# Kernel tuning notes

Hardware: AMD Instinct MI355X
Metric: run time of the kernel (lower is better)

## Reference

```python
import jax, jax.numpy as jnp
from jax import lax
import numpy as np

MARKER_NUM = 50000
E = 256          # embed_dim
D = 512          # d_model
K = 16           # sample_size / neighbor_num
B = 128
S = 128
BETA = 0.1
MAX_TIME = 1000.0


def setup_inputs() -> dict:
    key = jax.random.key(0)
    ks = jax.random.split(key, 12)
    def lin(k, fan_in, shape):
        return (jax.random.normal(k, shape, jnp.float32) / np.sqrt(fan_in)).astype(jnp.float32)
    return {
        "marker_data": jax.random.randint(ks[0], (B, S), 0, MARKER_NUM),
        "time_data": jax.random.uniform(ks[1], (B, S), jnp.float32),
        "mask_data": jnp.ones((B, S), jnp.float32),
        "embedding": jax.random.normal(ks[2], (MARKER_NUM, E), jnp.float32) * 0.05,
        "neighbor_list": jax.random.randint(ks[3], (MARKER_NUM, K), 0, MARKER_NUM),
        "neighbor_prob": jax.random.uniform(ks[4], (MARKER_NUM, K), jnp.float32),
        "W_te": lin(ks[5], 1, (1, E)), "b_te": jnp.zeros((E,), jnp.float32),
        "W_el": lin(ks[6], E, (E, D)), "b_el": jnp.zeros((D,), jnp.float32),
        "W_ih": lin(ks[7], D, (D, D)), "b_ih": jnp.zeros((D,), jnp.float32),
        "W_hh": lin(ks[8], D, (D, D)), "b_hh": jnp.zeros((D,), jnp.float32),
        "W_time": lin(ks[9], D, (D, 1)), "b_time": jnp.zeros((1,), jnp.float32),
        "W_mk": lin(ks[10], E + D, (E + D, 1)), "b_mk": jnp.zeros((1,), jnp.float32),
    }


def reference(marker_data, time_data, mask_data, embedding, neighbor_list, neighbor_prob,
              W_te, b_te, W_el, b_el, W_ih, b_ih, W_hh, b_hh, W_time, b_time, W_mk, b_mk):
    leaky = lambda x: jnp.where(x >= 0, x, 0.01 * x)  # LeakyReLU(0.01)
    Bn, Sn = marker_data.shape
    L = 1 + (Sn - 1) * (K - 1)  # final candidate_list / prob_list width
    R = 1 + (Sn - 1) * K        # final neighbor_prob_record width

    cand0 = jnp.zeros((Bn, L), jnp.int32).at[:, 0].set(marker_data[:, 0].astype(jnp.int32))
    prob0 = jnp.zeros((Bn, L), jnp.float32).at[:, 0].set(1.0)  # zero pad -> never sampled
    nrec0 = jnp.ones((Bn, R), jnp.float32)
    chosen0 = jnp.zeros((Bn, 1), jnp.int32)
    h0 = jnp.zeros((Bn, D), jnp.float32)
    carry0 = (h0, time_data[:, 0:1], marker_data[:, 0:1].astype(jnp.int32), cand0, prob0, nrec0, chosen0)
    keys = jax.random.split(jax.random.key(42), Sn - 1)

    def step(carry, xt):
        t, key = xt
        h, last_t, last_m, cand, prob, nrec, chosen = carry
        # embedding of (marker, time)
        time_emb = last_t @ W_te + b_te                       # (B,E)
        vec = embedding[last_m[:, 0]] + BETA * time_emb       # (B,E)
        x = leaky(vec @ W_el + b_el)                          # (B,D)
        # single-layer tanh RNN step (nn.RNN)
        h = jnp.tanh(x @ W_ih + b_ih + h @ W_hh + b_hh)
        new_t = last_t + jax.nn.softplus(h @ W_time + b_time)  # (B,1)
        new_mask = (new_t < MAX_TIME).astype(jnp.float32)
        # sampled neighbors of last marker
        neigh = neighbor_list[last_m[:, 0]].astype(jnp.int32)  # (B,K)
        p_neigh = neighbor_prob[last_m[:, 0]]                  # (B,K)
        nrec = lax.dynamic_update_slice(nrec, p_neigh, (0, 1 + t * K))
        inf = jnp.concatenate([embedding[neigh], jnp.broadcast_to(h[:, None, :], (Bn, K, D))], axis=-1)
        mprob = jax.nn.softmax((inf @ W_mk + b_mk)[..., 0], axis=1)  # (B,K)
        cand = lax.dynamic_update_slice(cand, neigh[:, 1:], (0, 1 + t * (K - 1)))
        chosen_p = jnp.take_along_axis(prob, chosen, 1)        # (B,1)
        attached = chosen_p * mprob                            # (B,K)
        prob = prob.at[jnp.arange(Bn), chosen[:, 0]].set(attached[:, 0])
        prob = lax.dynamic_update_slice(prob, attached[:, 1:], (0, 1 + t * (K - 1)))
        # torch.multinomial(prob_list, 1) == categorical over normalized probs
        logits = jnp.where(prob > 0, jnp.log(jnp.maximum(prob, 1e-38)), -1e30)
        new_chosen = jax.random.categorical(key, lax.stop_gradient(logits), axis=1)[:, None].astype(jnp.int32)
        new_m = jnp.take_along_axis(cand, new_chosen, 1)       # (B,1)
        sel_np = jnp.take_along_axis(nrec, new_chosen, 1)
        sel_sp = jnp.take_along_axis(prob, new_chosen, 1)
        new_carry = (h, new_t, new_m, cand, prob, nrec, new_chosen)
        return new_carry, (new_m[:, 0], new_t[:, 0], new_mask[:, 0], sel_np[:, 0], sel_sp[:, 0])

    _, (ms, ts, mk, nps, sps) = lax.scan(step, carry0, (jnp.arange(Sn - 1), keys))
    ones = jnp.ones((Bn, 1), jnp.float32)
    marker_res = jnp.concatenate([marker_data[:, 0:1].astype(jnp.int32), ms.T], axis=1)
    time_res = jnp.concatenate([time_data[:, 0:1], ts.T], axis=1)
    mask_res = jnp.concatenate([mask_data[:, 0:1], mk.T], axis=1)
    total_neighbor_prob = jnp.concatenate([ones, nps.T], axis=1)
    total_sample_prob = jnp.concatenate([ones, sps.T], axis=1)
    return (marker_res, time_res, mask_res, total_neighbor_prob, total_sample_prob)
```

## Files before the change

### kernel.cpp

```cpp
#include <hip/hip_runtime.h>
#include <stdint.h>
#include <stddef.h>

#define BB 128
#define SS 128
#define EE 256
#define DD 512
#define KK 16
#define LL 1906
#define RR 2033
#define NSTEP 127

static __device__ __forceinline__ uint32_t rotl32(uint32_t v, int r) {
  return (v << r) | (v >> (32 - r));
}

static __device__ __forceinline__ void tf2x32(uint32_t k0, uint32_t k1,
                                              uint32_t x0, uint32_t x1,
                                              uint32_t &o0, uint32_t &o1) {
  uint32_t ks2 = k0 ^ k1 ^ 0x1BD11BDAu;
  x0 += k0; x1 += k1;
#define TFR(r) { x0 += x1; x1 = rotl32(x1, (r)); x1 ^= x0; }
  TFR(13) TFR(15) TFR(26) TFR(6)
  x0 += k1;  x1 += ks2 + 1u;
  TFR(17) TFR(29) TFR(16) TFR(24)
  x0 += ks2; x1 += k0 + 2u;
  TFR(13) TFR(15) TFR(26) TFR(6)
  x0 += k0;  x1 += k1 + 3u;
  TFR(17) TFR(29) TFR(16) TFR(24)
  x0 += k1;  x1 += ks2 + 4u;
  TFR(13) TFR(15) TFR(26) TFR(6)
  x0 += ks2; x1 += k0 + 5u;
#undef TFR
  o0 = x0; o1 = x1;
}

static __device__ __forceinline__ float jax_gumbel(uint32_t bits) {
  float f = __uint_as_float((bits >> 9) | 0x3F800000u) - 1.0f;
  float u = fmaxf(f, 1.17549435e-38f);
  return -logf(-logf(u));
}

__global__ __launch_bounds__(1024) void rnn_gen_kernel(
    const int*   __restrict__ marker_data,
    const float* __restrict__ time_data,
    const float* __restrict__ mask_data,
    const float* __restrict__ embedding,
    const int*   __restrict__ neighbor_list,
    const float* __restrict__ neighbor_prob,
    const float* __restrict__ W_te,
    const float* __restrict__ b_te,
    const float* __restrict__ W_el,
    const float* __restrict__ b_el,
    const float* __restrict__ W_ih,
    const float* __restrict__ b_ih,
    const float* __restrict__ W_hh,
    const float* __restrict__ b_hh,
    const float* __restrict__ W_time,
    const float* __restrict__ b_time,
    const float* __restrict__ W_mk,
    const float* __restrict__ b_mk,
    float* __restrict__ out)
{
  __shared__ float  s_prob[LL];
  __shared__ int    s_cand[LL];
  __shared__ float  s_nrec[RR];
  __shared__ float  s_x[DD];
  __shared__ float  s_h[DD];
  __shared__ float  s_vec[EE];
  __shared__ double s_pd[8][DD];
  __shared__ double s_edot[KK];
  __shared__ double s_rt[8];
  __shared__ double s_rm[8];
  __shared__ float  s_red_z[16];
  __shared__ int    s_red_i[16];
  __shared__ int    s_neigh[KK];
  __shared__ float  s_last_t;
  __shared__ int    s_last_m;
  __shared__ int    s_chosen;
  __shared__ float  s_newt;
  __shared__ uint32_t s_k0, s_k1;

  const int b   = blockIdx.x;
  const int tid = threadIdx.x;

  for (int i = tid; i < LL; i += 1024) { s_prob[i] = 0.0f; s_cand[i] = 0; }
  for (int i = tid; i < RR; i += 1024) s_nrec[i] = 1.0f;
  if (tid < DD) s_h[tid] = 0.0f;
  if (tid == 0) {
    int   m0 = marker_data[b * SS];
    float t0 = time_data[b * SS];
    s_cand[0] = m0; s_prob[0] = 1.0f;
    s_last_m = m0; s_last_t = t0; s_chosen = 0;
    out[0 * BB * SS + b * SS + 0] = (float)m0;
    out[1 * BB * SS + b * SS + 0] = t0;
    out[2 * BB * SS + b * SS + 0] = mask_data[b * SS];
    out[3 * BB * SS + b * SS + 0] = 1.0f;
    out[4 * BB * SS + b * SS + 0] = 1.0f;
  }
  __syncthreads();

  for (int t = 0; t < NSTEP; ++t) {
    const int   m  = s_last_m;
    const float lt = s_last_t;

    if (tid == 768) {
      uint32_t o0, o1;
      tf2x32(0u, 42u, 0u, (uint32_t)t, o0, o1);
      s_k0 = o0; s_k1 = o1;
    }
    if (tid < EE) {
      float te = __fadd_rn(__fmul_rn(lt, W_te[tid]), b_te[tid]);
      s_vec[tid] = __fadd_rn(embedding[(size_t)m * EE + tid], __fmul_rn(0.1f, te));
    }
    if (tid >= 256 && tid < 256 + KK) {
      int k = tid - 256;
      int nb = neighbor_list[(size_t)m * KK + k];
      s_neigh[k] = nb;
      s_nrec[1 + t * KK + k] = neighbor_prob[(size_t)m * KK + k];
      if (k >= 1) s_cand[1 + t * (KK - 1) + (k - 1)] = nb;
    }
    __syncthreads();

    float4 ev0 = make_float4(0.f,0.f,0.f,0.f), ev1 = ev0;
    if (tid >= 512) {
      int k = (tid - 512) >> 5, l32 = tid & 31;
      const float4* er = (const float4*)(embedding + (size_t)s_neigh[k] * EE);
      ev0 = er[2 * l32]; ev1 = er[2 * l32 + 1];
    }
    {
      const int jg = tid & 127;
      const int i0 = (tid >> 7) << 5;
      const float4* W4 = (const float4*)W_el + (size_t)i0 * 128 + jg;
      double d0 = 0.0, d1 = 0.0, d2 = 0.0, d3 = 0.0;
#pragma unroll 4
      for (int i = 0; i < 32; i += 4) {
        float4 a4 = *(const float4*)&s_vec[i0 + i];
        float4 w0 = W4[0], w1 = W4[128], w2 = W4[256], w3 = W4[384];
        W4 += 512;
        d0 = fma((double)a4.x, (double)w0.x, d0); d1 = fma((double)a4.x, (double)w0.y, d1);
        d2 = fma((double)a4.x, (double)w0.z, d2); d3 = fma((double)a4.x, (double)w0.w, d3);
        d0 = fma((double)a4.y, (double)w1.x, d0); d1 = fma((double)a4.y, (double)w1.y, d1);
        d2 = fma((double)a4.y, (double)w1.z, d2); d3 = fma((double)a4.y, (double)w1.w, d3);
        d0 = fma((double)a4.z, (double)w2.x, d0); d1 = fma((double)a4.z, (double)w2.y, d1);
        d2 = fma((double)a4.z, (double)w2.z, d2); d3 = fma((double)a4.z, (double)w2.w, d3);
        d0 = fma((double)a4.w, (double)w3.x, d0); d1 = fma((double)a4.w, (double)w3.y, d1);
        d2 = fma((double)a4.w, (double)w3.z, d2); d3 = fma((double)a4.w, (double)w3.w, d3);
      }
      double* pd = &s_pd[tid >> 7][4 * jg];
      pd[0] = d0; pd[1] = d1; pd[2] = d2; pd[3] = d3;
    }
    __syncthreads();

    if (tid < DD) {
      double d = ((s_pd[0][tid] + s_pd[1][tid]) + (s_pd[2][tid] + s_pd[3][tid]))
               + ((s_pd[4][tid] + s_pd[5][tid]) + (s_pd[6][tid] + s_pd[7][tid]));
      float z = __fadd_rn((float)d, b_el[tid]);
      s_x[tid] = (z >= 0.0f) ? z : __fmul_rn(0.01f, z);
    }
    __syncthreads();

    {
      const int tl = tid & 511;
      const int jg = tl & 127;
      const int i0 = (tl >> 7) << 7;
      const float*  av = (tid < 512) ? s_x : s_h;
      const float*  Wm = (tid < 512) ? W_ih : W_hh;
      const float4* W4 = (const float4*)Wm + (size_t)i0 * 128 + jg;
      double d0 = 0.0, d1 = 0.0, d2 = 0.0, d3 = 0.0;
#pragma unroll 4
      for (int i = 0; i < 128; i += 4) {
        float4 a4 = *(const float4*)&av[i0 + i];
        float4 w0 = W4[0], w1 = W4[128], w2 = W4[256], w3 = W4[384];
        W4 += 512;
        d0 = fma((double)a4.x, (double)w0.x, d0); d1 = fma((double)a4.x, (double)w0.y, d1);
        d2 = fma((double)a4.x, (double)w0.z, d2); d3 = fma((double)a4.x, (double)w0.w, d3);
        d0 = fma((double)a4.y, (double)w1.x, d0); d1 = fma((double)a4.y, (double)w1.y, d1);
        d2 = fma((double)a4.y, (double)w1.z, d2); d3 = fma((double)a4.y, (double)w1.w, d3);
        d0 = fma((double)a4.z, (double)w2.x, d0); d1 = fma((double)a4.z, (double)w2.y, d1);
        d2 = fma((double)a4.z, (double)w2.z, d2); d3 = fma((double)a4.z, (double)w2.w, d3);
        d0 = fma((double)a4.w, (double)w3.x, d0); d1 = fma((double)a4.w, (double)w3.y, d1);
        d2 = fma((double)a4.w, (double)w3.z, d2); d3 = fma((double)a4.w, (double)w3.w, d3);
      }
      double* pd = &s_pd[tid >> 7][4 * jg];
      pd[0] = d0; pd[1] = d1; pd[2] = d2; pd[3] = d3;
    }
    __syncthreads();

    if (tid < DD) {
      double ih = (s_pd[0][tid] + s_pd[1][tid]) + (s_pd[2][tid] + s_pd[3][tid]);
      double hh = (s_pd[4][tid] + s_pd[5][tid]) + (s_pd[6][tid] + s_pd[7][tid]);
      float p = __fadd_rn(__fadd_rn(__fadd_rn((float)ih, b_ih[tid]), (float)hh), b_hh[tid]);
      s_h[tid] = (float)tanh((double)p);
    }
    __syncthreads();

    if (tid < DD) {
      double hv = (double)s_h[tid];
      double pt = hv * (double)W_time[tid];
      double pm = hv * (double)W_mk[EE + tid];
      for (int off = 32; off > 0; off >>= 1) {
        pt += __shfl_down(pt, off);
        pm += __shfl_down(pm, off);
      }
      if ((tid & 63) == 0) { s_rt[tid >> 6] = pt; s_rm[tid >> 6] = pm; }
    } else {
      int k = (tid - 512) >> 5, l32 = tid & 31, e0 = l32 * 8;
      const float4* wm4 = (const float4*)W_mk;
      float4 wm0 = wm4[2 * l32], wm1 = wm4[2 * l32 + 1];
      double acc = 0.0;
      acc = fma((double)ev0.x, (double)wm0.x, acc);
      acc = fma((double)ev0.y, (double)wm0.y, acc);
      acc = fma((double)ev0.z, (double)wm0.z, acc);
      acc = fma((double)ev0.w, (double)wm0.w, acc);
      acc = fma((double)ev1.x, (double)wm1.x, acc);
      acc = fma((double)ev1.y, (double)wm1.y, acc);
      acc = fma((double)ev1.z, (double)wm1.z, acc);
      acc = fma((double)ev1.w, (double)wm1.w, acc);
      (void)e0;
      for (int off = 16; off > 0; off >>= 1) acc += __shfl_down(acc, off, 32);
      if (l32 == 0) s_edot[k] = acc;
    }
    __syncthreads();

    if (tid < KK) {
      double hmk = ((s_rm[0] + s_rm[1]) + (s_rm[2] + s_rm[3]))
                 + ((s_rm[4] + s_rm[5]) + (s_rm[6] + s_rm[7]));
      float sc = __fadd_rn((float)(s_edot[tid] + hmk), b_mk[0]);
      float mx = sc;
      for (int k = 0; k < KK; ++k) mx = fmaxf(mx, __shfl(sc, k));
      float ee = expf(__fsub_rn(sc, mx));
      float ssum = 0.0f;
      for (int k = 0; k < KK; ++k) ssum = __fadd_rn(ssum, __shfl(ee, k));
      float cp = s_prob[s_chosen];
      float at = __fmul_rn(cp, __fdiv_rn(ee, ssum));
      if (tid == 0) s_prob[s_chosen] = at;
      else          s_prob[1 + t * (KK - 1) + (tid - 1)] = at;
    } else if (tid == 16) {
      double ht = ((s_rt[0] + s_rt[1]) + (s_rt[2] + s_rt[3]))
                + ((s_rt[4] + s_rt[5]) + (s_rt[6] + s_rt[7]));
      float td = __fadd_rn((float)ht, b_time[0]);
      float sp = __fadd_rn(fmaxf(td, 0.0f), log1pf(expf(-fabsf(td))));
      s_newt = __fadd_rn(s_last_t, sp);
    }
    __syncthreads();

    const int active = 16 + 15 * t;
    const uint32_t kk0 = s_k0, kk1 = s_k1;
    float bz = -3.0e38f;
    int   bi = 0x7FFFFFFF;
    for (int l = tid; l < active; l += 1024) {
      uint32_t i = (uint32_t)(b * LL + l);
      uint32_t o0, o1;
      tf2x32(kk0, kk1, 0u, i, o0, o1);
      float g  = jax_gumbel(o0 ^ o1);
      float pr = s_prob[l];
      float z  = (pr > 0.0f) ? __fadd_rn(logf(fmaxf(pr, 1e-38f)), g)
                             : __fadd_rn(-1e30f, g);
      if (z > bz) { bz = z; bi = l; }
    }
    for (int off = 32; off > 0; off >>= 1) {
      float oz = __shfl_down(bz, off);
      int   oi = __shfl_down(bi, off);
      if (oz > bz || (oz == bz && oi < bi)) { bz = oz; bi = oi; }
    }
    if ((tid & 63) == 0) { s_red_z[tid >> 6] = bz; s_red_i[tid >> 6] = bi; }
    __syncthreads();

    if (tid == 0) {
      float z0 = s_red_z[0]; int i0 = s_red_i[0];
      for (int w = 1; w < 16; ++w) {
        if (s_red_z[w] > z0 || (s_red_z[w] == z0 && s_red_i[w] < i0)) {
          z0 = s_red_z[w]; i0 = s_red_i[w];
        }
      }
      int   nm  = s_cand[i0];
      float np_ = s_nrec[i0];
      float sp_ = s_prob[i0];
      float nt  = s_newt;
      out[0 * BB * SS + b * SS + (t + 1)] = (float)nm;
      out[1 * BB * SS + b * SS + (t + 1)] = nt;
      out[2 * BB * SS + b * SS + (t + 1)] = (nt < 1000.0f) ? 1.0f : 0.0f;
      out[3 * BB * SS + b * SS + (t + 1)] = np_;
      out[4 * BB * SS + b * SS + (t + 1)] = sp_;
      s_chosen = i0; s_last_m = nm; s_last_t = nt;
    }
    __syncthreads();
  }
}

extern "C" void kernel_launch(void* const* d_in, const int* in_sizes, int n_in,
                              void* d_out, int out_size, void* d_ws, size_t ws_size,
                              hipStream_t stream) {
  (void)in_sizes; (void)n_in; (void)out_size; (void)d_ws; (void)ws_size;
  const int*   marker_data   = (const int*)  d_in[0];
  const float* time_data     = (const float*)d_in[1];
  const float* mask_data     = (const float*)d_in[2];
  const float* embedding     = (const float*)d_in[3];
  const int*   neighbor_list = (const int*)  d_in[4];
  const float* neighbor_prob = (const float*)d_in[5];
  const float* W_te   = (const float*)d_in[6];
  const float* b_te   = (const float*)d_in[7];
  const float* W_el   = (const float*)d_in[8];
  const float* b_el   = (const float*)d_in[9];
  const float* W_ih   = (const float*)d_in[10];
  const float* b_ih   = (const float*)d_in[11];
  const float* W_hh   = (const float*)d_in[12];
  const float* b_hh   = (const float*)d_in[13];
  const float* W_time = (const float*)d_in[14];
  const float* b_time = (const float*)d_in[15];
  const float* W_mk   = (const float*)d_in[16];
  const float* b_mk   = (const float*)d_in[17];
  float* out = (float*)d_out;

  hipLaunchKernelGGL(rnn_gen_kernel, dim3(BB), dim3(1024), 0, stream,
                     marker_data, time_data, mask_data, embedding,
                     neighbor_list, neighbor_prob,
                     W_te, b_te, W_el, b_el, W_ih, b_ih, W_hh, b_hh,
                     W_time, b_time, W_mk, b_mk, out);
}
```

Before: 3.542 ms.

## Overlap W_hh matvec with embedding projection and split ih across all threads

The recurrent W_hh·h product depends only on the previous hidden state, so it now runs in the same phase as the W_el embedding projection, written to a second partial-sum buffer. W_ih·x then runs on all 1024 threads with half the rows each instead of sharing the block with W_hh. The separate tanh pass is merged into the output-projection reduction, which removes one barrier. It costs an extra 32KB shared buffer of doubles and a launch_bounds occupancy hint; the reduction order for ih/hh changes from a 4-way to an 8-way split.

```diff
diff --git a/kernel.cpp b/kernel.cpp
--- a/kernel.cpp
+++ b/kernel.cpp
@@ -41,7 +41,7 @@
   return -logf(-logf(u));
 }
 
-__global__ __launch_bounds__(1024) void rnn_gen_kernel(
+__global__ __launch_bounds__(1024, 4) void rnn_gen_kernel(
     const int*   __restrict__ marker_data,
     const float* __restrict__ time_data,
     const float* __restrict__ mask_data,
@@ -62,16 +62,17 @@
     const float* __restrict__ b_mk,
     float* __restrict__ out)
 {
+  __shared__ double s_pd[8][DD];
+  __shared__ double s_pd2[8][DD];
+  __shared__ double s_edot[KK];
+  __shared__ double s_rt[8];
+  __shared__ double s_rm[8];
   __shared__ float  s_prob[LL];
   __shared__ int    s_cand[LL];
   __shared__ float  s_nrec[RR];
   __shared__ float  s_x[DD];
   __shared__ float  s_h[DD];
   __shared__ float  s_vec[EE];
-  __shared__ double s_pd[8][DD];
-  __shared__ double s_edot[KK];
-  __shared__ double s_rt[8];
-  __shared__ double s_rm[8];
   __shared__ float  s_red_z[16];
   __shared__ int    s_red_i[16];
   __shared__ int    s_neigh[KK];
@@ -128,9 +129,10 @@
       const float4* er = (const float4*)(embedding + (size_t)s_neigh[k] * EE);
       ev0 = er[2 * l32]; ev1 = er[2 * l32 + 1];
     }
+    const int jg = tid & 127;
+    const int sl = tid >> 7;
     {
-      const int jg = tid & 127;
-      const int i0 = (tid >> 7) << 5;
+      const int i0 = sl << 5;
       const float4* W4 = (const float4*)W_el + (size_t)i0 * 128 + jg;
       double d0 = 0.0, d1 = 0.0, d2 = 0.0, d3 = 0.0;
 #pragma unroll 4
@@ -147,30 +149,16 @@
         d0 = fma((double)a4.w, (double)w3.x, d0); d1 = fma((double)a4.w, (double)w3.y, d1);
         d2 = fma((double)a4.w, (double)w3.z, d2); d3 = fma((double)a4.w, (double)w3.w, d3);
       }
-      double* pd = &s_pd[tid >> 7][4 * jg];
+      double* pd = &s_pd[sl][4 * jg];
       pd[0] = d0; pd[1] = d1; pd[2] = d2; pd[3] = d3;
     }
-    __syncthreads();
-
-    if (tid < DD) {
-      double d = ((s_pd[0][tid] + s_pd[1][tid]) + (s_pd[2][tid] + s_pd[3][tid]))
-               + ((s_pd[4][tid] + s_pd[5][tid]) + (s_pd[6][tid] + s_pd[7][tid]));
-      float z = __fadd_rn((float)d, b_el[tid]);
-      s_x[tid] = (z >= 0.0f) ? z : __fmul_rn(0.01f, z);
-    }
-    __syncthreads();
-
     {
-      const int tl = tid & 511;
-      const int jg = tl & 127;
-      const int i0 = (tl >> 7) << 7;
-      const float*  av = (tid < 512) ? s_x : s_h;
-      const float*  Wm = (tid < 512) ? W_ih : W_hh;
-      const float4* W4 = (const float4*)Wm + (size_t)i0 * 128 + jg;
+      const int i0 = sl << 6;
+      const float4* W4 = (const float4*)W_hh + (size_t)i0 * 128 + jg;
       double d0 = 0.0, d1 = 0.0, d2 = 0.0, d3 = 0.0;
 #pragma unroll 4
-      for (int i = 0; i < 128; i += 4) {
-        float4 a4 = *(const float4*)&av[i0 + i];
+      for (int i = 0; i < 64; i += 4) {
+        float4 a4 = *(const float4*)&s_h[i0 + i];
         float4 w0 = W4[0], w1 = W4[128], w2 = W4[256], w3 = W4[384];
         W4 += 512;
         d0 = fma((double)a4.x, (double)w0.x, d0); d1 = fma((double)a4.x, (double)w0.y, d1);
@@ -182,21 +170,51 @@
         d0 = fma((double)a4.w, (double)w3.x, d0); d1 = fma((double)a4.w, (double)w3.y, d1);
         d2 = fma((double)a4.w, (double)w3.z, d2); d3 = fma((double)a4.w, (double)w3.w, d3);
       }
-      double* pd = &s_pd[tid >> 7][4 * jg];
+      double* pd = &s_pd2[sl][4 * jg];
       pd[0] = d0; pd[1] = d1; pd[2] = d2; pd[3] = d3;
     }
     __syncthreads();
 
     if (tid < DD) {
-      double ih = (s_pd[0][tid] + s_pd[1][tid]) + (s_pd[2][tid] + s_pd[3][tid]);
-      double hh = (s_pd[4][tid] + s_pd[5][tid]) + (s_pd[6][tid] + s_pd[7][tid]);
+      double d = ((s_pd[0][tid] + s_pd[1][tid]) + (s_pd[2][tid] + s_pd[3][tid]))
+               + ((s_pd[4][tid] + s_pd[5][tid]) + (s_pd[6][tid] + s_pd[7][tid]));
+      float z = __fadd_rn((float)d, b_el[tid]);
+      s_x[tid] = (z >= 0.0f) ? z : __fmul_rn(0.01f, z);
+    }
+    __syncthreads();
+
+    {
+      const int i0 = sl << 6;
+      const float4* W4 = (const float4*)W_ih + (size_t)i0 * 128 + jg;
+      double d0 = 0.0, d1 = 0.0, d2 = 0.0, d3 = 0.0;
+#pragma unroll 4
+      for (int i = 0; i < 64; i += 4) {
+        float4 a4 = *(const float4*)&s_x[i0 + i];
+        float4 w0 = W4[0], w1 = W4[128], w2 = W4[256], w3 = W4[384];
+        W4 += 512;
+        d0 = fma((double)a4.x, (double)w0.x, d0); d1 = fma((double)a4.x, (double)w0.y, d1);
+        d2 = fma((double)a4.x, (double)w0.z, d2); d3 = fma((double)a4.x, (double)w0.w, d3);
+        d0 = fma((double)a4.y, (double)w1.x, d0); d1 = fma((double)a4.y, (double)w1.y, d1);
+        d2 = fma((double)a4.y, (double)w1.z, d2); d3 = fma((double)a4.y, (double)w1.w, d3);
+        d0 = fma((double)a4.z, (double)w2.x, d0); d1 = fma((double)a4.z, (double)w2.y, d1);
+        d2 = fma((double)a4.z, (double)w2.z, d2); d3 = fma((double)a4.z, (double)w2.w, d3);
+        d0 = fma((double)a4.w, (double)w3.x, d0); d1 = fma((double)a4.w, (double)w3.y, d1);
+        d2 = fma((double)a4.w, (double)w3.z, d2); d3 = fma((double)a4.w, (double)w3.w, d3);
+      }
+      double* pd = &s_pd[sl][4 * jg];
+      pd[0] = d0; pd[1] = d1; pd[2] = d2; pd[3] = d3;
+    }
+    __syncthreads();
+
+    if (tid < DD) {
+      double ih = ((s_pd[0][tid] + s_pd[1][tid]) + (s_pd[2][tid] + s_pd[3][tid]))
+                + ((s_pd[4][tid] + s_pd[5][tid]) + (s_pd[6][tid] + s_pd[7][tid]));
+      double hh = ((s_pd2[0][tid] + s_pd2[1][tid]) + (s_pd2[2][tid] + s_pd2[3][tid]))
+                + ((s_pd2[4][tid] + s_pd2[5][tid]) + (s_pd2[6][tid] + s_pd2[7][tid]));
       float p = __fadd_rn(__fadd_rn(__fadd_rn((float)ih, b_ih[tid]), (float)hh), b_hh[tid]);
-      s_h[tid] = (float)tanh((double)p);
-    }
-    __syncthreads();
-
-    if (tid < DD) {
-      double hv = (double)s_h[tid];
+      float hf = (float)tanh((double)p);
+      s_h[tid] = hf;
+      double hv = (double)hf;
       double pt = hv * (double)W_time[tid];
       double pm = hv * (double)W_mk[EE + tid];
       for (int off = 32; off > 0; off >>= 1) {
@@ -205,7 +223,7 @@
       }
       if ((tid & 63) == 0) { s_rt[tid >> 6] = pt; s_rm[tid >> 6] = pm; }
     } else {
-      int k = (tid - 512) >> 5, l32 = tid & 31, e0 = l32 * 8;
+      int k = (tid - 512) >> 5, l32 = tid & 31;
       const float4* wm4 = (const float4*)W_mk;
       float4 wm0 = wm4[2 * l32], wm1 = wm4[2 * l32 + 1];
       double acc = 0.0;
@@ -217,7 +235,6 @@
       acc = fma((double)ev1.y, (double)wm1.y, acc);
       acc = fma((double)ev1.z, (double)wm1.z, acc);
       acc = fma((double)ev1.w, (double)wm1.w, acc);
-      (void)e0;
       for (int off = 16; off > 0; off >>= 1) acc += __shfl_down(acc, off, 32);
       if (l32 == 0) s_edot[k] = acc;
     }
```

New measurement: 3.713 ms. 1.05x slower.

## Overlap next-step W_hh matvec with sampling via split warp groups and partial barriers

Applied to the files above, without the earlier changes.

Splits the 1024-thread block into two halves after the hidden update. The upper 512 threads compute the next step's W_hh·h product, while the lower 512 run the score, softmax, Gumbel sampling and next-embedding prep, synchronising among themselves with a shared-memory atomic counter barrier instead of __syncthreads. It also caches log-probabilities so the sampling loop no longer calls logf per candidate, and moves the neighbor-embedding dot product to the end of the previous step. The spin barrier and the extra shared memory add risk of hangs or lower occupancy, and the matvec loops switch from float4 to float2 loads.

```diff
diff --git a/kernel.cpp b/kernel.cpp
--- a/kernel.cpp
+++ b/kernel.cpp
@@ -41,249 +41,288 @@
   return -logf(-logf(u));
 }
 
-__global__ __launch_bounds__(1024) void rnn_gen_kernel(
+static __device__ __forceinline__ void s_bar8(int* ctr, int tgt) {
+  __threadfence_block();
+  if ((threadIdx.x & 63) == 0)
+    __hip_atomic_fetch_add(ctr, 1, __ATOMIC_RELAXED, __HIP_MEMORY_SCOPE_WORKGROUP);
+  while (__hip_atomic_load(ctr, __ATOMIC_RELAXED, __HIP_MEMORY_SCOPE_WORKGROUP) < tgt) {}
+  __threadfence_block();
+}
+
+__global__ __launch_bounds__(1024, 4) void rnn_gen_kernel(
     const int*   __restrict__ marker_data,
     const float* __restrict__ time_data,
     const float* __restrict__ mask_data,
     const float* __restrict__ embedding,
     const int*   __restrict__ neighbor_list,
     const float* __restrict__ neighbor_prob,
-    const float* __restrict__ W_te,
-    const float* __restrict__ b_te,
-    const float* __restrict__ W_el,
-    const float* __restrict__ b_el,
-    const float* __restrict__ W_ih,
-    const float* __restrict__ b_ih,
-    const float* __restrict__ W_hh,
-    const float* __restrict__ b_hh,
-    const float* __restrict__ W_time,
-    const float* __restrict__ b_time,
-    const float* __restrict__ W_mk,
-    const float* __restrict__ b_mk,
+    const float* __restrict__ W_te, const float* __restrict__ b_te,
+    const float* __restrict__ W_el, const float* __restrict__ b_el,
+    const float* __restrict__ W_ih, const float* __restrict__ b_ih,
+    const float* __restrict__ W_hh, const float* __restrict__ b_hh,
+    const float* __restrict__ W_time, const float* __restrict__ b_time,
+    const float* __restrict__ W_mk, const float* __restrict__ b_mk,
     float* __restrict__ out)
 {
+  __shared__ double s_pdA[4][DD];
+  __shared__ double s_pdB[2][DD];
   __shared__ float  s_prob[LL];
+  __shared__ float  s_logp[LL];
   __shared__ int    s_cand[LL];
   __shared__ float  s_nrec[RR];
+  __shared__ float  s_vec[EE];
   __shared__ float  s_x[DD];
   __shared__ float  s_h[DD];
-  __shared__ float  s_vec[EE];
-  __shared__ double s_pd[8][DD];
   __shared__ double s_edot[KK];
   __shared__ double s_rt[8];
   __shared__ double s_rm[8];
-  __shared__ float  s_red_z[16];
-  __shared__ int    s_red_i[16];
+  __shared__ float  s_red_z[8];
+  __shared__ int    s_red_i[8];
   __shared__ int    s_neigh[KK];
   __shared__ float  s_last_t;
   __shared__ int    s_last_m;
   __shared__ int    s_chosen;
   __shared__ float  s_newt;
   __shared__ uint32_t s_k0, s_k1;
+  __shared__ int    s_ctr;
 
   const int b   = blockIdx.x;
   const int tid = threadIdx.x;
 
-  for (int i = tid; i < LL; i += 1024) { s_prob[i] = 0.0f; s_cand[i] = 0; }
+  for (int i = tid; i < LL; i += 1024) { s_prob[i] = 0.0f; s_logp[i] = -1e30f; s_cand[i] = 0; }
   for (int i = tid; i < RR; i += 1024) s_nrec[i] = 1.0f;
   if (tid < DD) s_h[tid] = 0.0f;
+  if (tid < 2 * DD) ((double*)s_pdB)[tid] = 0.0;
   if (tid == 0) {
+    s_ctr = 0;
     int   m0 = marker_data[b * SS];
     float t0 = time_data[b * SS];
-    s_cand[0] = m0; s_prob[0] = 1.0f;
+    s_cand[0] = m0; s_prob[0] = 1.0f; s_logp[0] = 0.0f;
     s_last_m = m0; s_last_t = t0; s_chosen = 0;
-    out[0 * BB * SS + b * SS + 0] = (float)m0;
-    out[1 * BB * SS + b * SS + 0] = t0;
-    out[2 * BB * SS + b * SS + 0] = mask_data[b * SS];
-    out[3 * BB * SS + b * SS + 0] = 1.0f;
-    out[4 * BB * SS + b * SS + 0] = 1.0f;
+    out[0 * BB * SS + b * SS] = (float)m0;
+    out[1 * BB * SS + b * SS] = t0;
+    out[2 * BB * SS + b * SS] = mask_data[b * SS];
+    out[3 * BB * SS + b * SS] = 1.0f;
+    out[4 * BB * SS + b * SS] = 1.0f;
   }
   __syncthreads();
 
-  for (int t = 0; t < NSTEP; ++t) {
+  {
     const int   m  = s_last_m;
     const float lt = s_last_t;
-
-    if (tid == 768) {
-      uint32_t o0, o1;
-      tf2x32(0u, 42u, 0u, (uint32_t)t, o0, o1);
-      s_k0 = o0; s_k1 = o1;
-    }
     if (tid < EE) {
       float te = __fadd_rn(__fmul_rn(lt, W_te[tid]), b_te[tid]);
       s_vec[tid] = __fadd_rn(embedding[(size_t)m * EE + tid], __fmul_rn(0.1f, te));
     }
-    if (tid >= 256 && tid < 256 + KK) {
-      int k = tid - 256;
+    if (tid >= 256 && tid < 512) {
+      int k = (tid - 256) >> 4, l16 = tid & 15;
       int nb = neighbor_list[(size_t)m * KK + k];
-      s_neigh[k] = nb;
-      s_nrec[1 + t * KK + k] = neighbor_prob[(size_t)m * KK + k];
-      if (k >= 1) s_cand[1 + t * (KK - 1) + (k - 1)] = nb;
-    }
-    __syncthreads();
-
-    float4 ev0 = make_float4(0.f,0.f,0.f,0.f), ev1 = ev0;
-    if (tid >= 512) {
-      int k = (tid - 512) >> 5, l32 = tid & 31;
-      const float4* er = (const float4*)(embedding + (size_t)s_neigh[k] * EE);
-      ev0 = er[2 * l32]; ev1 = er[2 * l32 + 1];
-    }
+      if (l16 == 0) {
+        s_neigh[k] = nb;
+        s_nrec[1 + 0 * KK + k] = neighbor_prob[(size_t)m * KK + k];
+        if (k >= 1) s_cand[1 + 0 * (KK - 1) + (k - 1)] = nb;
+      }
+      const float4* er = (const float4*)(embedding + (size_t)nb * EE) + 4 * l16;
+      const float4* wm = (const float4*)W_mk + 4 * l16;
+      float4 e0 = er[0], e1 = er[1], e2 = er[2], e3 = er[3];
+      float4 m0_ = wm[0], m1_ = wm[1], m2_ = wm[2], m3_ = wm[3];
+      double acc = 0.0;
+      acc = fma((double)e0.x, (double)m0_.x, acc); acc = fma((double)e0.y, (double)m0_.y, acc);
+      acc = fma((double)e0.z, (double)m0_.z, acc); acc = fma((double)e0.w, (double)m0_.w, acc);
+      acc = fma((double)e1.x, (double)m1_.x, acc); acc = fma((double)e1.y, (double)m1_.y, acc);
+      acc = fma((double)e1.z, (double)m1_.z, acc); acc = fma((double)e1.w, (double)m1_.w, acc);
+      acc = fma((double)e2.x, (double)m2_.x, acc); acc = fma((double)e2.y, (double)m2_.y, acc);
+      acc = fma((double)e2.z, (double)m2_.z, acc); acc = fma((double)e2.w, (double)m2_.w, acc);
+      acc = fma((double)e3.x, (double)m3_.x, acc); acc = fma((double)e3.y, (double)m3_.y, acc);
+      acc = fma((double)e3.z, (double)m3_.z, acc); acc = fma((double)e3.w, (double)m3_.w, acc);
+      for (int off = 8; off > 0; off >>= 1) acc += __shfl_down(acc, off, 16);
+      if (l16 == 0) s_edot[k] = acc;
+    }
+  }
+  __syncthreads();
+
+  int sep = 0;
+  const int jg2 = tid & 255;
+  const int slA = tid >> 8;
+
+  for (int t = 0; t < NSTEP; ++t) {
     {
-      const int jg = tid & 127;
-      const int i0 = (tid >> 7) << 5;
-      const float4* W4 = (const float4*)W_el + (size_t)i0 * 128 + jg;
-      double d0 = 0.0, d1 = 0.0, d2 = 0.0, d3 = 0.0;
-#pragma unroll 4
-      for (int i = 0; i < 32; i += 4) {
-        float4 a4 = *(const float4*)&s_vec[i0 + i];
-        float4 w0 = W4[0], w1 = W4[128], w2 = W4[256], w3 = W4[384];
-        W4 += 512;
-        d0 = fma((double)a4.x, (double)w0.x, d0); d1 = fma((double)a4.x, (double)w0.y, d1);
-        d2 = fma((double)a4.x, (double)w0.z, d2); d3 = fma((double)a4.x, (double)w0.w, d3);
-        d0 = fma((double)a4.y, (double)w1.x, d0); d1 = fma((double)a4.y, (double)w1.y, d1);
-        d2 = fma((double)a4.y, (double)w1.z, d2); d3 = fma((double)a4.y, (double)w1.w, d3);
-        d0 = fma((double)a4.z, (double)w2.x, d0); d1 = fma((double)a4.z, (double)w2.y, d1);
-        d2 = fma((double)a4.z, (double)w2.z, d2); d3 = fma((double)a4.z, (double)w2.w, d3);
-        d0 = fma((double)a4.w, (double)w3.x, d0); d1 = fma((double)a4.w, (double)w3.y, d1);
-        d2 = fma((double)a4.w, (double)w3.z, d2); d3 = fma((double)a4.w, (double)w3.w, d3);
-      }
-      double* pd = &s_pd[tid >> 7][4 * jg];
-      pd[0] = d0; pd[1] = d1; pd[2] = d2; pd[3] = d3;
+      const int i0 = slA << 6;
+      const float2* W2 = (const float2*)W_el + (size_t)i0 * 256 + jg2;
+      double a0 = 0.0, a1 = 0.0;
+#pragma unroll 8
+      for (int i = 0; i < 64; ++i) {
+        float2 w = W2[(size_t)i * 256];
+        double v = (double)s_vec[i0 + i];
+        a0 = fma(v, (double)w.x, a0);
+        a1 = fma(v, (double)w.y, a1);
+      }
+      s_pdA[slA][2 * jg2] = a0; s_pdA[slA][2 * jg2 + 1] = a1;
     }
     __syncthreads();
 
     if (tid < DD) {
-      double d = ((s_pd[0][tid] + s_pd[1][tid]) + (s_pd[2][tid] + s_pd[3][tid]))
-               + ((s_pd[4][tid] + s_pd[5][tid]) + (s_pd[6][tid] + s_pd[7][tid]));
+      double d = (s_pdA[0][tid] + s_pdA[1][tid]) + (s_pdA[2][tid] + s_pdA[3][tid]);
       float z = __fadd_rn((float)d, b_el[tid]);
       s_x[tid] = (z >= 0.0f) ? z : __fmul_rn(0.01f, z);
     }
     __syncthreads();
 
     {
-      const int tl = tid & 511;
-      const int jg = tl & 127;
-      const int i0 = (tl >> 7) << 7;
-      const float*  av = (tid < 512) ? s_x : s_h;
-      const float*  Wm = (tid < 512) ? W_ih : W_hh;
-      const float4* W4 = (const float4*)Wm + (size_t)i0 * 128 + jg;
-      double d0 = 0.0, d1 = 0.0, d2 = 0.0, d3 = 0.0;
-#pragma unroll 4
-      for (int i = 0; i < 128; i += 4) {
-        float4 a4 = *(const float4*)&av[i0 + i];
-        float4 w0 = W4[0], w1 = W4[128], w2 = W4[256], w3 = W4[384];
-        W4 += 512;
-        d0 = fma((double)a4.x, (double)w0.x, d0); d1 = fma((double)a4.x, (double)w0.y, d1);
-        d2 = fma((double)a4.x, (double)w0.z, d2); d3 = fma((double)a4.x, (double)w0.w, d3);
-        d0 = fma((double)a4.y, (double)w1.x, d0); d1 = fma((double)a4.y, (double)w1.y, d1);
-        d2 = fma((double)a4.y, (double)w1.z, d2); d3 = fma((double)a4.y, (double)w1.w, d3);
-        d0 = fma((double)a4.z, (double)w2.x, d0); d1 = fma((double)a4.z, (double)w2.y, d1);
-        d2 = fma((double)a4.z, (double)w2.z, d2); d3 = fma((double)a4.z, (double)w2.w, d3);
-        d0 = fma((double)a4.w, (double)w3.x, d0); d1 = fma((double)a4.w, (double)w3.y, d1);
-        d2 = fma((double)a4.w, (double)w3.z, d2); d3 = fma((double)a4.w, (double)w3.w, d3);
-      }
-      double* pd = &s_pd[tid >> 7][4 * jg];
-      pd[0] = d0; pd[1] = d1; pd[2] = d2; pd[3] = d3;
+      const int i0 = slA << 7;
+      const float2* W2 = (const float2*)W_ih + (size_t)i0 * 256 + jg2;
+      double a0 = 0.0, a1 = 0.0;
+#pragma unroll 8
+      for (int i = 0; i < 128; ++i) {
+        float2 w = W2[(size_t)i * 256];
+        double v = (double)s_x[i0 + i];
+        a0 = fma(v, (double)w.x, a0);
+        a1 = fma(v, (double)w.y, a1);
+      }
+      s_pdA[slA][2 * jg2] = a0; s_pdA[slA][2 * jg2 + 1] = a1;
     }
     __syncthreads();
 
     if (tid < DD) {
-      double ih = (s_pd[0][tid] + s_pd[1][tid]) + (s_pd[2][tid] + s_pd[3][tid]);
-      double hh = (s_pd[4][tid] + s_pd[5][tid]) + (s_pd[6][tid] + s_pd[7][tid]);
+      double ih = (s_pdA[0][tid] + s_pdA[1][tid]) + (s_pdA[2][tid] + s_pdA[3][tid]);
+      double hh = s_pdB[0][tid] + s_pdB[1][tid];
       float p = __fadd_rn(__fadd_rn(__fadd_rn((float)ih, b_ih[tid]), (float)hh), b_hh[tid]);
       s_h[tid] = (float)tanh((double)p);
     }
     __syncthreads();
 
-    if (tid < DD) {
-      double hv = (double)s_h[tid];
-      double pt = hv * (double)W_time[tid];
-      double pm = hv * (double)W_mk[EE + tid];
-      for (int off = 32; off > 0; off >>= 1) {
-        pt += __shfl_down(pt, off);
-        pm += __shfl_down(pm, off);
-      }
-      if ((tid & 63) == 0) { s_rt[tid >> 6] = pt; s_rm[tid >> 6] = pm; }
+    if (tid >= 512) {
+      if (t + 1 < NSTEP) {
+        const int q  = tid - 512;
+        const int j2 = q & 255;
+        const int sl = q >> 8;
+        const int i0 = sl << 8;
+        const float2* W2 = (const float2*)W_hh + (size_t)i0 * 256 + j2;
+        double a0 = 0.0, a1 = 0.0;
+#pragma unroll 8
+        for (int i = 0; i < 256; ++i) {
+          float2 w = W2[(size_t)i * 256];
+          double v = (double)s_h[i0 + i];
+          a0 = fma(v, (double)w.x, a0);
+          a1 = fma(v, (double)w.y, a1);
+        }
+        s_pdB[sl][2 * j2] = a0; s_pdB[sl][2 * j2 + 1] = a1;
+      }
     } else {
-      int k = (tid - 512) >> 5, l32 = tid & 31, e0 = l32 * 8;
-      const float4* wm4 = (const float4*)W_mk;
-      float4 wm0 = wm4[2 * l32], wm1 = wm4[2 * l32 + 1];
-      double acc = 0.0;
-      acc = fma((double)ev0.x, (double)wm0.x, acc);
-      acc = fma((double)ev0.y, (double)wm0.y, acc);
-      acc = fma((double)ev0.z, (double)wm0.z, acc);
-      acc = fma((double)ev0.w, (double)wm0.w, acc);
-      acc = fma((double)ev1.x, (double)wm1.x, acc);
-      acc = fma((double)ev1.y, (double)wm1.y, acc);
-      acc = fma((double)ev1.z, (double)wm1.z, acc);
-      acc = fma((double)ev1.w, (double)wm1.w, acc);
-      (void)e0;
-      for (int off = 16; off > 0; off >>= 1) acc += __shfl_down(acc, off, 32);
-      if (l32 == 0) s_edot[k] = acc;
-    }
-    __syncthreads();
-
-    if (tid < KK) {
-      double hmk = ((s_rm[0] + s_rm[1]) + (s_rm[2] + s_rm[3]))
-                 + ((s_rm[4] + s_rm[5]) + (s_rm[6] + s_rm[7]));
-      float sc = __fadd_rn((float)(s_edot[tid] + hmk), b_mk[0]);
-      float mx = sc;
-      for (int k = 0; k < KK; ++k) mx = fmaxf(mx, __shfl(sc, k));
-      float ee = expf(__fsub_rn(sc, mx));
-      float ssum = 0.0f;
-      for (int k = 0; k < KK; ++k) ssum = __fadd_rn(ssum, __shfl(ee, k));
-      float cp = s_prob[s_chosen];
-      float at = __fmul_rn(cp, __fdiv_rn(ee, ssum));
-      if (tid == 0) s_prob[s_chosen] = at;
-      else          s_prob[1 + t * (KK - 1) + (tid - 1)] = at;
-    } else if (tid == 16) {
-      double ht = ((s_rt[0] + s_rt[1]) + (s_rt[2] + s_rt[3]))
-                + ((s_rt[4] + s_rt[5]) + (s_rt[6] + s_rt[7]));
-      float td = __fadd_rn((float)ht, b_time[0]);
-      float sp = __fadd_rn(fmaxf(td, 0.0f), log1pf(expf(-fabsf(td))));
-      s_newt = __fadd_rn(s_last_t, sp);
-    }
-    __syncthreads();
-
-    const int active = 16 + 15 * t;
-    const uint32_t kk0 = s_k0, kk1 = s_k1;
-    float bz = -3.0e38f;
-    int   bi = 0x7FFFFFFF;
-    for (int l = tid; l < active; l += 1024) {
-      uint32_t i = (uint32_t)(b * LL + l);
-      uint32_t o0, o1;
-      tf2x32(kk0, kk1, 0u, i, o0, o1);
-      float g  = jax_gumbel(o0 ^ o1);
-      float pr = s_prob[l];
-      float z  = (pr > 0.0f) ? __fadd_rn(logf(fmaxf(pr, 1e-38f)), g)
-                             : __fadd_rn(-1e30f, g);
-      if (z > bz) { bz = z; bi = l; }
-    }
-    for (int off = 32; off > 0; off >>= 1) {
-      float oz = __shfl_down(bz, off);
-      int   oi = __shfl_down(bi, off);
-      if (oz > bz || (oz == bz && oi < bi)) { bz = oz; bi = oi; }
-    }
-    if ((tid & 63) == 0) { s_red_z[tid >> 6] = bz; s_red_i[tid >> 6] = bi; }
-    __syncthreads();
-
-    if (tid == 0) {
-      float z0 = s_red_z[0]; int i0 = s_red_i[0];
-      for (int w = 1; w < 16; ++w) {
-        if (s_red_z[w] > z0 || (s_red_z[w] == z0 && s_red_i[w] < i0)) {
-          z0 = s_red_z[w]; i0 = s_red_i[w];
-        }
-      }
-      int   nm  = s_cand[i0];
-      float np_ = s_nrec[i0];
-      float sp_ = s_prob[i0];
-      float nt  = s_newt;
-      out[0 * BB * SS + b * SS + (t + 1)] = (float)nm;
-      out[1 * BB * SS + b * SS + (t + 1)] = nt;
-      out[2 * BB * SS + b * SS + (t + 1)] = (nt < 1000.0f) ? 1.0f : 0.0f;
-      out[3 * BB * SS + b * SS + (t + 1)] = np_;
-      out[4 * BB * SS + b * SS + (t + 1)] = sp_;
-      s_chosen = i0; s_last_m = nm; s_last_t = nt;
+      {
+        double hv = (double)s_h[tid];
+        double pt = hv * (double)W_time[tid];
+        double pm = hv * (double)W_mk[EE + tid];
+        for (int off = 32; off > 0; off >>= 1) {
+          pt += __shfl_down(pt, off);
+          pm += __shfl_down(pm, off);
+        }
+        if ((tid & 63) == 0) { s_rt[tid >> 6] = pt; s_rm[tid >> 6] = pm; }
+      }
+      ++sep; s_bar8(&s_ctr, 8 * sep);
+
+      if (tid < KK) {
+        double hmk = ((s_rm[0] + s_rm[1]) + (s_rm[2] + s_rm[3]))
+                   + ((s_rm[4] + s_rm[5]) + (s_rm[6] + s_rm[7]));
+        float sc = __fadd_rn((float)(s_edot[tid] + hmk), b_mk[0]);
+        float mx = sc;
+        for (int k = 0; k < KK; ++k) mx = fmaxf(mx, __shfl(sc, k));
+        float ee = expf(__fsub_rn(sc, mx));
+        float ssum = 0.0f;
+        for (int k = 0; k < KK; ++k) ssum = __fadd_rn(ssum, __shfl(ee, k));
+        float cp = s_prob[s_chosen];
+        float at = __fmul_rn(cp, __fdiv_rn(ee, ssum));
+        float lp = (at > 0.0f) ? logf(fmaxf(at, 1e-38f)) : -1e30f;
+        if (tid == 0) { s_prob[s_chosen] = at; s_logp[s_chosen] = lp; }
+        else {
+          int idx = 1 + t * (KK - 1) + (tid - 1);
+          s_prob[idx] = at; s_logp[idx] = lp;
+        }
+      } else if (tid == 16) {
+        double ht = ((s_rt[0] + s_rt[1]) + (s_rt[2] + s_rt[3]))
+                  + ((s_rt[4] + s_rt[5]) + (s_rt[6] + s_rt[7]));
+        float td = __fadd_rn((float)ht, b_time[0]);
+        float sp = __fadd_rn(fmaxf(td, 0.0f), log1pf(expf(-fabsf(td))));
+        s_newt = __fadd_rn(s_last_t, sp);
+      } else if (tid == 17) {
+        uint32_t o0, o1;
+        tf2x32(0u, 42u, 0u, (uint32_t)t, o0, o1);
+        s_k0 = o0; s_k1 = o1;
+      }
+      ++sep; s_bar8(&s_ctr, 8 * sep);
+
+      {
+        const int active = 16 + 15 * t;
+        const uint32_t kk0 = s_k0, kk1 = s_k1;
+        float bz = -3.0e38f;
+        int   bi = 0x7FFFFFFF;
+        for (int l = tid; l < active; l += 512) {
+          uint32_t i = (uint32_t)(b * LL + l);
+          uint32_t o0, o1;
+          tf2x32(kk0, kk1, 0u, i, o0, o1);
+          float g = jax_gumbel(o0 ^ o1);
+          float z = __fadd_rn(s_logp[l], g);
+          if (z > bz) { bz = z; bi = l; }
+        }
+        for (int off = 32; off > 0; off >>= 1) {
+          float oz = __shfl_down(bz, off);
+          int   oi = __shfl_down(bi, off);
+          if (oz > bz || (oz == bz && oi < bi)) { bz = oz; bi = oi; }
+        }
+        if ((tid & 63) == 0) { s_red_z[tid >> 6] = bz; s_red_i[tid >> 6] = bi; }
+      }
+      ++sep; s_bar8(&s_ctr, 8 * sep);
+
+      if (tid == 0) {
+        float z0 = s_red_z[0]; int i0 = s_red_i[0];
+        for (int w = 1; w < 8; ++w) {
+          if (s_red_z[w] > z0 || (s_red_z[w] == z0 && s_red_i[w] < i0)) {
+            z0 = s_red_z[w]; i0 = s_red_i[w];
+          }
+        }
+        int   nm = s_cand[i0];
+        float nt = s_newt;
+        out[0 * BB * SS + b * SS + (t + 1)] = (float)nm;
+        out[1 * BB * SS + b * SS + (t + 1)] = nt;
+        out[2 * BB * SS + b * SS + (t + 1)] = (nt < 1000.0f) ? 1.0f : 0.0f;
+        out[3 * BB * SS + b * SS + (t + 1)] = s_nrec[i0];
+        out[4 * BB * SS + b * SS + (t + 1)] = s_prob[i0];
+        s_chosen = i0; s_last_m = nm; s_last_t = nt;
+      }
+      ++sep; s_bar8(&s_ctr, 8 * sep);
+
+      if (t + 1 < NSTEP) {
+        const int   m   = s_last_m;
+        const float lt2 = s_last_t;
+        if (tid < EE) {
+          float te = __fadd_rn(__fmul_rn(lt2, W_te[tid]), b_te[tid]);
+          s_vec[tid] = __fadd_rn(embedding[(size_t)m * EE + tid], __fmul_rn(0.1f, te));
+        }
+        if (tid >= 256) {
+          int k = (tid - 256) >> 4, l16 = tid & 15;
+          int nb = neighbor_list[(size_t)m * KK + k];
+          if (l16 == 0) {
+            s_neigh[k] = nb;
+            s_nrec[1 + (t + 1) * KK + k] = neighbor_prob[(size_t)m * KK + k];
+            if (k >= 1) s_cand[1 + (t + 1) * (KK - 1) + (k - 1)] = nb;
+          }
+          const float4* er = (const float4*)(embedding + (size_t)nb * EE) + 4 * l16;
+          const float4* wm = (const float4*)W_mk + 4 * l16;
+          float4 e0 = er[0], e1 = er[1], e2 = er[2], e3 = er[3];
+          float4 m0_ = wm[0], m1_ = wm[1], m2_ = wm[2], m3_ = wm[3];
+          double acc = 0.0;
+          acc = fma((double)e0.x, (double)m0_.x, acc); acc = fma((double)e0.y, (double)m0_.y, acc);
+          acc = fma((double)e0.z, (double)m0_.z, acc); acc = fma((double)e0.w, (double)m0_.w, acc);
+          acc = fma((double)e1.x, (double)m1_.x, acc); acc = fma((double)e1.y, (double)m1_.y, acc);
+          acc = fma((double)e1.z, (double)m1_.z, acc); acc = fma((double)e1.w, (double)m1_.w, acc);
+          acc = fma((double)e2.x, (double)m2_.x, acc); acc = fma((double)e2.y, (double)m2_.y, acc);
+          acc = fma((double)e2.z, (double)m2_.z, acc); acc = fma((double)e2.w, (double)m2_.w, acc);
+          acc = fma((double)e3.x, (double)m3_.x, acc); acc = fma((double)e3.y, (double)m3_.y, acc);
+          acc = fma((double)e3.z, (double)m3_.z, acc); acc = fma((double)e3.w, (double)m3_.w, acc);
+          for (int off = 8; off > 0; off >>= 1) acc += __shfl_down(acc, off, 16);
+          if (l16 == 0) s_edot[k] = acc;
+        }
+      }
     }
     __syncthreads();
   }
```

Result: slower. 6.097 ms (+72.1%).
